# Optimization experiments

Hardware: AMD Instinct MI355X
Metric: run time of the kernel (lower is better)

## Reference

```python
import jax, jax.numpy as jnp
import numpy as np

N, FDIM, HDIM, STEPS = 8192, 512, 1024, 50
STRESS, QNOISE = 0.0, 0.1


def setup_inputs() -> dict:
    key = jax.random.key(0)
    ks = jax.random.split(key, 20)
    s = 0.02
    d = {
        "real_antigen": jax.random.normal(ks[0], (N, FDIM), jnp.float32),
        "steps": STEPS,
        # quantum gene projection (self-loop graph -> per-node linear)
        "Wq": jax.random.normal(ks[1], (FDIM, HDIM), jnp.float32) * s,
        "bq": jnp.zeros((HDIM,), jnp.float32),
        # denoise_0: Linear(h,h) ReLU Linear(h,f)
        "W01": jax.random.normal(ks[2], (HDIM, HDIM), jnp.float32) * s,
        "b01": jnp.zeros((HDIM,), jnp.float32),
        "W02": jax.random.normal(ks[3], (HDIM, FDIM), jnp.float32) * s,
        "b02": jnp.zeros((FDIM,), jnp.float32),
        # denoise_1: Linear(h,h) Tanh Linear(h,f)
        "W11": jax.random.normal(ks[4], (HDIM, HDIM), jnp.float32) * s,
        "b11": jnp.zeros((HDIM,), jnp.float32),
        "W12": jax.random.normal(ks[5], (HDIM, FDIM), jnp.float32) * s,
        "b12": jnp.zeros((FDIM,), jnp.float32),
        # interference_net: Linear(2f,h) GELU Linear(h,f)
        "Wi1": jax.random.normal(ks[6], (2 * FDIM, HDIM), jnp.float32) * s,
        "bi1": jnp.zeros((HDIM,), jnp.float32),
        "Wi2": jax.random.normal(ks[7], (HDIM, FDIM), jnp.float32) * s,
        "bi2": jnp.zeros((FDIM,), jnp.float32),
        # quantum state scalars
        "alpha_amp": jnp.asarray(np.cos(0.6), jnp.float32),
        "beta_amp": jnp.asarray(np.sin(0.6), jnp.float32),
        "phase_cos": jnp.asarray(np.cos(0.3), jnp.float32),
    }
    return d


def reference(real_antigen, steps, Wq, bq, W01, b01, W02, b02, W11, b11,
              W12, b12, Wi1, bi1, Wi2, bi2, alpha_amp, beta_amp, phase_cos):
    sched = jnp.linspace(1e-4, 0.02, 100, dtype=jnp.float32)
    decoherence_rate = jnp.float32(0.1 + STRESS * 0.5)
    decay = jnp.exp(-decoherence_rate)
    # quantum probabilities (fixed amplitudes during the rollout)
    a2, b2 = alpha_amp ** 2, beta_amp ** 2
    p0 = a2 / (a2 + b2)
    p1 = b2 / (a2 + b2)
    sp0, sp1 = jnp.sqrt(p0), jnp.sqrt(p1)
    base_key = jax.random.key(1)
    x0 = jax.random.normal(jax.random.fold_in(base_key, 10_000), real_antigen.shape, jnp.float32)

    def step(carry, t):
        x, coh = carry
        qf = jax.nn.relu(x @ Wq + bq)                           # [N, H]
        d0 = jax.nn.relu(qf @ W01 + b01) @ W02 + b02            # [N, F]
        d1 = jnp.tanh(qf @ W11 + b11) @ W12 + b12               # [N, F]
        inter_in = jnp.concatenate([d0, d1], axis=-1)           # [N, 2F]
        interf = jax.nn.gelu(inter_in @ Wi1 + bi1, approximate=False) @ Wi2 + bi2
        qi = 2.0 * jnp.sqrt(p0 * p1) * phase_cos * coh          # scalar interference
        denoised = sp0 * d0 + sp1 * d1 + qi * interf
        alpha = jnp.maximum(1.0 - sched[t], 1e-8)
        alpha_prev = jnp.where(t > 0, 1.0 - sched[jnp.maximum(t - 1, 0)], 1.0)
        sqrt_1ma = jnp.sqrt(jnp.maximum(1.0 - alpha, 1e-8))
        x_new = (x - (1.0 - alpha) / sqrt_1ma * denoised) / jnp.sqrt(alpha)
        sigma = jnp.sqrt(jnp.maximum((1.0 - alpha_prev) / (1.0 - alpha) * (1.0 - alpha / alpha_prev), 0.0))
        noise = jax.random.normal(jax.random.fold_in(base_key, t), x.shape, jnp.float32)
        x_new = jnp.where(t > 0, x_new + (sigma + QNOISE * jnp.abs(qi)) * noise, x_new)
        return (x_new, coh * decay), None

    ts = jnp.arange(int(steps) - 1, -1, -1, dtype=jnp.int32)
    (x, _), _ = jax.lax.scan(step, (x0, jnp.float32(1.0)), ts)
    # quantum measurement: collapse to |0> with probability p0
    u = jax.random.uniform(jax.random.fold_in(base_key, 99_999), (), jnp.float32)
    dream = jnp.where(u < p0, 0.7 * x + 0.3 * real_antigen, x)
    return dream
```

## Files before the change

kernel.cpp:

```cpp
#include <hip/hip_runtime.h>
#include <stdint.h>
#include <math.h>


typedef __bf16 bf16x8 __attribute__((ext_vector_type(8)));
typedef float floatx4 __attribute__((ext_vector_type(4)));

__host__ __device__ inline void tf2x32(uint32_t k0, uint32_t k1,
                                       uint32_t x0, uint32_t x1,
                                       uint32_t& o0, uint32_t& o1) {
  uint32_t ks2 = k0 ^ k1 ^ 0x1BD11BDAu;
#define TF_R(r) { x0 += x1; x1 = (x1 << (r)) | (x1 >> (32 - (r))); x1 ^= x0; }
  x0 += k0; x1 += k1;
  TF_R(13) TF_R(15) TF_R(26) TF_R(6)
  x0 += k1;  x1 += ks2 + 1u;
  TF_R(17) TF_R(29) TF_R(16) TF_R(24)
  x0 += ks2; x1 += k0 + 2u;
  TF_R(13) TF_R(15) TF_R(26) TF_R(6)
  x0 += k0;  x1 += k1 + 3u;
  TF_R(17) TF_R(29) TF_R(16) TF_R(24)
  x0 += k1;  x1 += ks2 + 4u;
  TF_R(13) TF_R(15) TF_R(26) TF_R(6)
  x0 += ks2; x1 += k0 + 5u;
#undef TF_R
  o0 = x0; o1 = x1;
}

__device__ inline float erfinv_f32(float x) {
  float w = -log1pf(-x * x);
  float p;
  if (w < 5.0f) {
    w = w - 2.5f;
    p = 2.81022636e-08f;
    p = fmaf(p, w, 3.43273939e-07f);
    p = fmaf(p, w, -3.5233877e-06f);
    p = fmaf(p, w, -4.39150654e-06f);
    p = fmaf(p, w, 0.00021858087f);
    p = fmaf(p, w, -0.00125372503f);
    p = fmaf(p, w, -0.00417768164f);
    p = fmaf(p, w, 0.246640727f);
    p = fmaf(p, w, 1.50140941f);
  } else {
    w = sqrtf(w) - 3.0f;
    p = -0.000200214257f;
    p = fmaf(p, w, 0.000100950558f);
    p = fmaf(p, w, 0.00134934322f);
    p = fmaf(p, w, -0.00367342844f);
    p = fmaf(p, w, 0.00573950773f);
    p = fmaf(p, w, -0.0076224613f);
    p = fmaf(p, w, 0.00943887047f);
    p = fmaf(p, w, 1.00167406f);
    p = fmaf(p, w, 2.83297682f);
  }
  return p * x;
}

__device__ inline float tf_normal(uint32_t k0, uint32_t k1, uint32_t i) {
  uint32_t o0, o1;
  tf2x32(k0, k1, 0u, i, o0, o1);
  uint32_t bits = o0 ^ o1;
  float f = __uint_as_float(0x3F800000u | (bits >> 9)) - 1.0f;
  float u = f * 2.0f + (-0.99999994f);
  u = fmaxf(-0.99999994f, u);
  return 1.41421356f * erfinv_f32(u);
}

__device__ inline unsigned short f2bf(float f) {
  uint32_t u = __float_as_uint(f);
  u += 0x7FFFu + ((u >> 16) & 1u);
  return (unsigned short)(u >> 16);
}
__device__ inline float bf2f(unsigned short h) {
  return __uint_as_float(((uint32_t)h) << 16);
}

__global__ __launch_bounds__(256)
void transpose_bf16_kernel(const float* __restrict__ W,
                           unsigned short* __restrict__ Wt, int K, int N) {
  __shared__ float tile[32][33];
  int kb = blockIdx.x * 32, nb = blockIdx.y * 32;
  int tx = threadIdx.x & 31, ty = threadIdx.x >> 5;
#pragma unroll
  for (int i = 0; i < 32; i += 8)
    tile[ty + i][tx] = W[(size_t)(kb + ty + i) * N + nb + tx];
  __syncthreads();
#pragma unroll
  for (int i = 0; i < 32; i += 8)
    Wt[(size_t)(nb + ty + i) * K + kb + tx] = f2bf(tile[tx][ty + i]);
}

__device__ __forceinline__ void gemm_core_db(
    const unsigned short* __restrict__ A0, const unsigned short* __restrict__ A1,
    int lda0, int lda1, int K0, int Ktot,
    const unsigned short* __restrict__ Bt,
    int row0, int col0,
    unsigned short (*As)[128 * 32], unsigned short (*Bs)[128 * 32],
    floatx4 (&acc)[4][4]) {
  const int tid = threadIdx.x;
  const int wave = tid >> 6, lane = tid & 63;
  const int wr = wave >> 1, wc = wave & 1;
  const int lrow = lane >> 2;
  const int lk = (lane & 3) * 8;
  const int fm = lane & 15, quad = lane >> 4;

  auto issue = [&](int kt, int buf) {
    const int k0 = kt * 32;
    const unsigned short* Ap; int kOff, lda;
    if (k0 < K0) { Ap = A0; kOff = k0; lda = lda0; }
    else         { Ap = A1; kOff = k0 - K0; lda = lda1; }
#pragma unroll
    for (int r = 0; r < 2; r++) {
      int srow = r * 64 + wave * 16 + lrow;
      __builtin_amdgcn_global_load_lds(
          (const __attribute__((address_space(1))) uint32_t*)
              (Ap + (size_t)(row0 + srow) * lda + kOff + lk),
          (__attribute__((address_space(3))) uint32_t*)(&As[buf][srow * 32 + lk]),
          16, 0, 0);
      __builtin_amdgcn_global_load_lds(
          (const __attribute__((address_space(1))) uint32_t*)
              (Bt + (size_t)(col0 + srow) * Ktot + k0 + lk),
          (__attribute__((address_space(3))) uint32_t*)(&Bs[buf][srow * 32 + lk]),
          16, 0, 0);
    }
  };

  const int nk = Ktot >> 5;
  issue(0, 0);
  for (int k = 0; k < nk; k++) {
    const int cur = k & 1;
    if (k + 1 < nk) {
      issue(k + 1, cur ^ 1);
      asm volatile("s_waitcnt vmcnt(4)\ns_barrier" ::: "memory");
    } else {
      asm volatile("s_waitcnt vmcnt(0)\ns_barrier" ::: "memory");
    }
    bf16x8 a[4], b[4];
#pragma unroll
    for (int u = 0; u < 4; u++)
      a[u] = *(const bf16x8*)(&As[cur][(wr * 64 + u * 16 + fm) * 32 + quad * 8]);
#pragma unroll
    for (int v = 0; v < 4; v++)
      b[v] = *(const bf16x8*)(&Bs[cur][(wc * 64 + v * 16 + fm) * 32 + quad * 8]);
#pragma unroll
    for (int u = 0; u < 4; u++)
#pragma unroll
      for (int v = 0; v < 4; v++)
        acc[u][v] = __builtin_amdgcn_mfma_f32_16x16x32_bf16(a[u], b[v],
                                                            acc[u][v], 0, 0, 0);
    asm volatile("s_barrier" ::: "memory");
  }
}

__device__ __forceinline__ void swizzled_block(int& row0, int& col0) {
  int id = blockIdx.x + gridDim.x * blockIdx.y;
  row0 = (id & 63) << 7;
  col0 = (id >> 6) << 7;
}

template<int ACT>
__global__ __launch_bounds__(256)
void mfma_gemm(const unsigned short* __restrict__ A0,
               const unsigned short* __restrict__ A1,
               int lda0, int lda1, int K0, int Ktot,
               const unsigned short* __restrict__ Bt,
               const float* __restrict__ bias0,
               const float* __restrict__ bias1, int nsplit,
               unsigned short* __restrict__ C0,
               unsigned short* __restrict__ C1, int ldc) {
  __shared__ unsigned short As[2][128 * 32];
  __shared__ unsigned short Bs[2][128 * 32];
  int row0, col0;
  swizzled_block(row0, col0);
  floatx4 acc[4][4];
#pragma unroll
  for (int u = 0; u < 4; u++)
#pragma unroll
    for (int v = 0; v < 4; v++) acc[u][v] = (floatx4){0.f, 0.f, 0.f, 0.f};
  gemm_core_db(A0, A1, lda0, lda1, K0, Ktot, Bt, row0, col0, As, Bs, acc);

  const int lane = threadIdx.x & 63, wave = threadIdx.x >> 6;
  const int wr = wave >> 1, wc = wave & 1;
  const int fm = lane & 15, quad = lane >> 4;
  const bool side = (ACT == 4) && (col0 >= nsplit);
  const float* bias = side ? bias1 : bias0;
  unsigned short* C = side ? C1 : C0;
  const int cbase = col0 - (side ? nsplit : 0);
#pragma unroll
  for (int v = 0; v < 4; v++) {
    int col = cbase + wc * 64 + v * 16 + fm;
    float bv = bias[col];
#pragma unroll
    for (int u = 0; u < 4; u++) {
      int rbase = row0 + wr * 64 + u * 16 + quad * 4;
#pragma unroll
      for (int r = 0; r < 4; r++) {
        float val = acc[u][v][r] + bv;
        if (ACT == 1) val = fmaxf(val, 0.0f);
        if (ACT == 2) val = tanhf(val);
        if (ACT == 3) val = 0.5f * val * (1.0f + erff(val * 0.70710678118654752f));
        if (ACT == 4) val = side ? tanhf(val) : fmaxf(val, 0.0f);
        C[(size_t)(rbase + r) * ldc + col] = f2bf(val);
      }
    }
  }
}

__global__ __launch_bounds__(256)
void mfma_gemm_pair(const unsigned short* __restrict__ Aa,
                    const unsigned short* __restrict__ Ab,
                    const unsigned short* __restrict__ Bta,
                    const unsigned short* __restrict__ Btb,
                    const float* __restrict__ biasa,
                    const float* __restrict__ biasb,
                    unsigned short* __restrict__ Ca,
                    unsigned short* __restrict__ Cb,
                    int Ktot, int ldc) {
  __shared__ unsigned short As[2][128 * 32];
  __shared__ unsigned short Bs[2][128 * 32];
  const int z = blockIdx.z;
  const unsigned short* A = z ? Ab : Aa;
  const unsigned short* Bt = z ? Btb : Bta;
  const float* bias = z ? biasb : biasa;
  unsigned short* C = z ? Cb : Ca;
  int row0, col0;
  swizzled_block(row0, col0);
  floatx4 acc[4][4];
#pragma unroll
  for (int u = 0; u < 4; u++)
#pragma unroll
    for (int v = 0; v < 4; v++) acc[u][v] = (floatx4){0.f, 0.f, 0.f, 0.f};
  gemm_core_db(A, A, Ktot, Ktot, Ktot, Ktot, Bt, row0, col0, As, Bs, acc);

  const int lane = threadIdx.x & 63, wave = threadIdx.x >> 6;
  const int wr = wave >> 1, wc = wave & 1;
  const int fm = lane & 15, quad = lane >> 4;
#pragma unroll
  for (int v = 0; v < 4; v++) {
    int col = col0 + wc * 64 + v * 16 + fm;
    float bv = bias[col];
#pragma unroll
    for (int u = 0; u < 4; u++) {
      int rbase = row0 + wr * 64 + u * 16 + quad * 4;
#pragma unroll
      for (int r = 0; r < 4; r++)
        C[(size_t)(rbase + r) * ldc + col] = f2bf(acc[u][v][r] + bv);
    }
  }
}

__global__ void init_normal_kernel(float* __restrict__ x,
                                   unsigned short* __restrict__ xbf,
                                   uint32_t k0, uint32_t k1, int n) {
  int i = blockIdx.x * blockDim.x + threadIdx.x;
  if (i >= n) return;
  float v = tf_normal(k0, k1, (uint32_t)i);
  x[i] = v;
  xbf[i] = f2bf(v);
}

__global__ void update_kernel(float* __restrict__ x,
                              unsigned short* __restrict__ xbf,
                              const unsigned short* __restrict__ d0,
                              const unsigned short* __restrict__ d1,
                              const unsigned short* __restrict__ itf,
                              const float* __restrict__ a_amp,
                              const float* __restrict__ b_amp,
                              const float* __restrict__ ph,
                              float coh, float c1, float sqrt_alpha,
                              float sigma, int add_noise,
                              uint32_t k0, uint32_t k1, int n) {
  int i = blockIdx.x * blockDim.x + threadIdx.x;
  if (i >= n) return;
  float aa = a_amp[0], bb = b_amp[0], pc = ph[0];
  float a2 = aa * aa, b2 = bb * bb, s = a2 + b2;
  float p0 = a2 / s, p1 = b2 / s;
  float qi = 2.0f * sqrtf(p0 * p1) * pc * coh;
  float den = sqrtf(p0) * bf2f(d0[i]) + sqrtf(p1) * bf2f(d1[i])
            + qi * bf2f(itf[i]);
  float xn = (x[i] - c1 * den) / sqrt_alpha;
  if (add_noise) {
    float nz = tf_normal(k0, k1, (uint32_t)i);
    xn += (sigma + 0.1f * fabsf(qi)) * nz;
  }
  x[i] = xn;
  xbf[i] = f2bf(xn);
}

__global__ void final_kernel(const float* __restrict__ x,
                             const float* __restrict__ real,
                             float* __restrict__ out,
                             const float* __restrict__ a_amp,
                             const float* __restrict__ b_amp,
                             uint32_t k0, uint32_t k1, int n) {
  int i = blockIdx.x * blockDim.x + threadIdx.x;
  if (i >= n) return;
  float aa = a_amp[0], bb = b_amp[0];
  float a2 = aa * aa, b2 = bb * bb;
  float p0 = a2 / (a2 + b2);
  uint32_t o0, o1;
  tf2x32(k0, k1, 0u, 0u, o0, o1);
  uint32_t bits = o0 ^ o1;
  float u = __uint_as_float(0x3F800000u | (bits >> 9)) - 1.0f;
  float xv = x[i];
  out[i] = (u < p0) ? (0.7f * xv + 0.3f * real[i]) : xv;
}

extern "C" void kernel_launch(void* const* d_in, const int* in_sizes, int n_in,
                              void* d_out, int out_size, void* d_ws,
                              size_t ws_size, hipStream_t stream) {
  const float* real = (const float*)d_in[0];
  const float* Wq  = (const float*)d_in[2];
  const float* bq  = (const float*)d_in[3];
  const float* W01 = (const float*)d_in[4];
  const float* b01 = (const float*)d_in[5];
  const float* W02 = (const float*)d_in[6];
  const float* b02 = (const float*)d_in[7];
  const float* W11 = (const float*)d_in[8];
  const float* b11 = (const float*)d_in[9];
  const float* W12 = (const float*)d_in[10];
  const float* b12 = (const float*)d_in[11];
  const float* Wi1 = (const float*)d_in[12];
  const float* bi1 = (const float*)d_in[13];
  const float* Wi2 = (const float*)d_in[14];
  const float* bi2 = (const float*)d_in[15];
  const float* a_amp = (const float*)d_in[16];
  const float* b_amp = (const float*)d_in[17];
  const float* ph    = (const float*)d_in[18];

  const int Nn = 8192, F = 512, H = 1024;
  const int nElem = Nn * F;
  const int NSPLIT_OFF = 1 << 30;

  char* ws = (char*)d_ws;
  float* x = (float*)ws;                                   ws += (size_t)nElem * 4;
  unsigned short* xbf = (unsigned short*)ws;               ws += (size_t)nElem * 2;
  unsigned short* qf  = (unsigned short*)ws;               ws += (size_t)Nn * H * 2;
  unsigned short* h0  = (unsigned short*)ws;               ws += (size_t)Nn * H * 2;
  unsigned short* h1  = (unsigned short*)ws;               ws += (size_t)Nn * H * 2;
  unsigned short* d0  = (unsigned short*)ws;               ws += (size_t)nElem * 2;
  unsigned short* d1  = (unsigned short*)ws;               ws += (size_t)nElem * 2;
  unsigned short* itf = (unsigned short*)ws;               ws += (size_t)nElem * 2;
  unsigned short* Wq_t  = (unsigned short*)ws;             ws += (size_t)F * H * 2;
  unsigned short* WA_t  = (unsigned short*)ws;             ws += (size_t)(2 * H) * H * 2;
  unsigned short* W02_t = (unsigned short*)ws;             ws += (size_t)H * F * 2;
  unsigned short* W12_t = (unsigned short*)ws;             ws += (size_t)H * F * 2;
  unsigned short* Wi1_t = (unsigned short*)ws;             ws += (size_t)(2 * F) * H * 2;
  unsigned short* Wi2_t = (unsigned short*)ws;             ws += (size_t)H * F * 2;

  dim3 tb(256);
  transpose_bf16_kernel<<<dim3(F / 32, H / 32), tb, 0, stream>>>(Wq, Wq_t, F, H);
  transpose_bf16_kernel<<<dim3(H / 32, H / 32), tb, 0, stream>>>(W01, WA_t, H, H);
  transpose_bf16_kernel<<<dim3(H / 32, H / 32), tb, 0, stream>>>(W11, WA_t + (size_t)H * H, H, H);
  transpose_bf16_kernel<<<dim3(H / 32, F / 32), tb, 0, stream>>>(W02, W02_t, H, F);
  transpose_bf16_kernel<<<dim3(H / 32, F / 32), tb, 0, stream>>>(W12, W12_t, H, F);
  transpose_bf16_kernel<<<dim3(2 * F / 32, H / 32), tb, 0, stream>>>(Wi1, Wi1_t, 2 * F, H);
  transpose_bf16_kernel<<<dim3(H / 32, F / 32), tb, 0, stream>>>(Wi2, Wi2_t, H, F);

  uint32_t kx0, kx1; tf2x32(0u, 1u, 0u, 10000u, kx0, kx1);
  init_normal_kernel<<<(nElem + 255) / 256, 256, 0, stream>>>(x, xbf, kx0, kx1, nElem);

  float sched[100];
  for (int i = 0; i < 100; i++)
    sched[i] = (float)(1e-4 + (0.02 - 1e-4) * (double)i / 99.0);
  const float decay = expf(-0.1f);
  float coh = 1.0f;

  dim3 blk(256);
  dim3 g1(H / 128, 64);
  dim3 g2(2 * H / 128, 64);
  dim3 g45(F / 128, 64, 2);
  dim3 g6(H / 128, 64);
  dim3 g7(F / 128, 64);

  for (int j = 0; j < 50; j++) {
    int t = 49 - j;
    mfma_gemm<1><<<g1, blk, 0, stream>>>(xbf, xbf, F, F, F, F, Wq_t,
                                         bq, nullptr, NSPLIT_OFF, qf, nullptr, H);
    mfma_gemm<4><<<g2, blk, 0, stream>>>(qf, qf, H, H, H, H, WA_t,
                                         b01, b11, H, h0, h1, H);
    mfma_gemm_pair<<<g45, blk, 0, stream>>>(h0, h1, W02_t, W12_t, b02, b12,
                                            d0, d1, H, F);
    mfma_gemm<3><<<g6, blk, 0, stream>>>(d0, d1, F, F, F, 2 * F, Wi1_t,
                                         bi1, nullptr, NSPLIT_OFF, qf, nullptr, H);
    mfma_gemm<0><<<g7, blk, 0, stream>>>(qf, qf, H, H, H, H, Wi2_t,
                                         bi2, nullptr, NSPLIT_OFF, itf, nullptr, F);

    float schedt = sched[t];
    float alphaf = fmaxf(1.0f - schedt, 1e-8f);
    float one_m_alpha = 1.0f - alphaf;
    float sqrt_1ma = sqrtf(fmaxf(one_m_alpha, 1e-8f));
    float c1 = one_m_alpha / sqrt_1ma;
    float sqa = sqrtf(alphaf);
    float sigma = 0.0f;
    if (t > 0) {
      float ap = 1.0f - sched[t - 1];
      sigma = sqrtf(fmaxf((1.0f - ap) / one_m_alpha * (1.0f - alphaf / ap), 0.0f));
    }
    uint32_t kt0, kt1; tf2x32(0u, 1u, 0u, (uint32_t)t, kt0, kt1);
    update_kernel<<<(nElem + 255) / 256, 256, 0, stream>>>(
        x, xbf, d0, d1, itf, a_amp, b_amp, ph, coh, c1, sqa, sigma,
        (t > 0) ? 1 : 0, kt0, kt1, nElem);
    coh *= decay;
  }

  uint32_t ku0, ku1; tf2x32(0u, 1u, 0u, 99999u, ku0, ku1);
  final_kernel<<<(nElem + 255) / 256, 256, 0, stream>>>(
      x, real, (float*)d_out, a_amp, b_amp, ku0, ku1, nElem);
}
```

Measured before the change: 9.416 ms.

## Fuse final interference GEMM with the diffusion update epilogue

The last GEMM of each step (Wi2) now applies the denoise/update math directly in its epilogue, so the separate elementwise update kernel and the bf16 itf buffer are removed. The MFMA operand order is swapped so each lane holds four consecutive columns of one row. That lets the epilogue use vectorized loads and stores of x, d0, d1 and xbf. This saves one launch and a full round trip of the interference tensor per step, but the GEMM epilogue now carries the Threefry normal generation, which adds register pressure and ALU work to that kernel.

```diff
diff --git a/kernel.cpp b/kernel.cpp
--- a/kernel.cpp
+++ b/kernel.cpp
@@ -5,6 +5,7 @@
 
 typedef __bf16 bf16x8 __attribute__((ext_vector_type(8)));
 typedef float floatx4 __attribute__((ext_vector_type(4)));
+typedef unsigned int uintx2 __attribute__((ext_vector_type(2)));
 
 __host__ __device__ inline void tf2x32(uint32_t k0, uint32_t k1,
                                        uint32_t x0, uint32_t x1,
@@ -73,6 +74,16 @@
 __device__ inline float bf2f(unsigned short h) {
   return __uint_as_float(((uint32_t)h) << 16);
 }
+__device__ inline uintx2 pack4bf(float a, float b, float c, float d) {
+  uintx2 r;
+  r.x = (uint32_t)f2bf(a) | ((uint32_t)f2bf(b) << 16);
+  r.y = (uint32_t)f2bf(c) | ((uint32_t)f2bf(d) << 16);
+  return r;
+}
+__device__ inline float bfx(uintx2 p, int r) {
+  uint32_t w = (r < 2) ? p.x : p.y;
+  return bf2f((unsigned short)((r & 1) ? (w >> 16) : (w & 0xffffu)));
+}
 
 __global__ __launch_bounds__(256)
 void transpose_bf16_kernel(const float* __restrict__ W,
@@ -89,6 +100,7 @@
     Wt[(size_t)(nb + ty + i) * K + kb + tx] = f2bf(tile[tx][ty + i]);
 }
 
+template<bool SWAP>
 __device__ __forceinline__ void gemm_core_db(
     const unsigned short* __restrict__ A0, const unsigned short* __restrict__ A1,
     int lda0, int lda1, int K0, int Ktot,
@@ -141,12 +153,21 @@
 #pragma unroll
     for (int v = 0; v < 4; v++)
       b[v] = *(const bf16x8*)(&Bs[cur][(wc * 64 + v * 16 + fm) * 32 + quad * 8]);
-#pragma unroll
-    for (int u = 0; u < 4; u++)
+    if constexpr (!SWAP) {
+#pragma unroll
+      for (int u = 0; u < 4; u++)
+#pragma unroll
+        for (int v = 0; v < 4; v++)
+          acc[u][v] = __builtin_amdgcn_mfma_f32_16x16x32_bf16(a[u], b[v],
+                                                              acc[u][v], 0, 0, 0);
+    } else {
 #pragma unroll
       for (int v = 0; v < 4; v++)
-        acc[u][v] = __builtin_amdgcn_mfma_f32_16x16x32_bf16(a[u], b[v],
-                                                            acc[u][v], 0, 0, 0);
+#pragma unroll
+        for (int u = 0; u < 4; u++)
+          acc[v][u] = __builtin_amdgcn_mfma_f32_16x16x32_bf16(b[v], a[u],
+                                                              acc[v][u], 0, 0, 0);
+    }
     asm volatile("s_barrier" ::: "memory");
   }
 }
@@ -176,7 +197,7 @@
   for (int u = 0; u < 4; u++)
 #pragma unroll
     for (int v = 0; v < 4; v++) acc[u][v] = (floatx4){0.f, 0.f, 0.f, 0.f};
-  gemm_core_db(A0, A1, lda0, lda1, K0, Ktot, Bt, row0, col0, As, Bs, acc);
+  gemm_core_db<false>(A0, A1, lda0, lda1, K0, Ktot, Bt, row0, col0, As, Bs, acc);
 
   const int lane = threadIdx.x & 63, wave = threadIdx.x >> 6;
   const int wr = wave >> 1, wc = wave & 1;
@@ -229,7 +250,7 @@
   for (int u = 0; u < 4; u++)
 #pragma unroll
     for (int v = 0; v < 4; v++) acc[u][v] = (floatx4){0.f, 0.f, 0.f, 0.f};
-  gemm_core_db(A, A, Ktot, Ktot, Ktot, Ktot, Bt, row0, col0, As, Bs, acc);
+  gemm_core_db<false>(A, A, Ktot, Ktot, Ktot, Ktot, Bt, row0, col0, As, Bs, acc);
 
   const int lane = threadIdx.x & 63, wave = threadIdx.x >> 6;
   const int wr = wave >> 1, wc = wave & 1;
@@ -244,6 +265,69 @@
 #pragma unroll
       for (int r = 0; r < 4; r++)
         C[(size_t)(rbase + r) * ldc + col] = f2bf(acc[u][v][r] + bv);
+    }
+  }
+}
+
+__global__ __launch_bounds__(256)
+void mfma_gemm_update(const unsigned short* __restrict__ A,
+                      const unsigned short* __restrict__ Bt,
+                      const float* __restrict__ bias,
+                      const unsigned short* __restrict__ d0,
+                      const unsigned short* __restrict__ d1,
+                      float* __restrict__ x,
+                      unsigned short* __restrict__ xbf,
+                      const float* __restrict__ a_amp,
+                      const float* __restrict__ b_amp,
+                      const float* __restrict__ ph,
+                      float coh, float c1, float sqa, float sigma,
+                      int add_noise, uint32_t k0, uint32_t k1) {
+  __shared__ unsigned short As[2][128 * 32];
+  __shared__ unsigned short Bs[2][128 * 32];
+  int row0, col0;
+  swizzled_block(row0, col0);
+  floatx4 acc[4][4];
+#pragma unroll
+  for (int v = 0; v < 4; v++)
+#pragma unroll
+    for (int u = 0; u < 4; u++) acc[v][u] = (floatx4){0.f, 0.f, 0.f, 0.f};
+  gemm_core_db<true>(A, A, 1024, 1024, 1024, 1024, Bt, row0, col0, As, Bs, acc);
+
+  float aa = a_amp[0], bb = b_amp[0], pc = ph[0];
+  float a2 = aa * aa, b2 = bb * bb, s = a2 + b2;
+  float p0 = a2 / s, p1 = b2 / s;
+  float sp0 = sqrtf(p0), sp1 = sqrtf(p1);
+  float qi = 2.0f * sqrtf(p0 * p1) * pc * coh;
+  float nscale = sigma + 0.1f * fabsf(qi);
+  float inv_sqa = 1.0f / sqa;
+
+  const int lane = threadIdx.x & 63, wave = threadIdx.x >> 6;
+  const int wr = wave >> 1, wc = wave & 1;
+  const int fm = lane & 15, quad = lane >> 4;
+  const int cbase = col0 + wc * 64 + quad * 4;
+#pragma unroll
+  for (int v = 0; v < 4; v++) {
+    int colb = cbase + v * 16;
+    floatx4 bv = *(const floatx4*)(bias + colb);
+#pragma unroll
+    for (int u = 0; u < 4; u++) {
+      int row = row0 + wr * 64 + u * 16 + fm;
+      size_t base = (size_t)row * 512 + colb;
+      uintx2 d0p = *(const uintx2*)(d0 + base);
+      uintx2 d1p = *(const uintx2*)(d1 + base);
+      floatx4 xv = *(const floatx4*)(x + base);
+      floatx4 xn;
+#pragma unroll
+      for (int r = 0; r < 4; r++) {
+        float itf = acc[v][u][r] + bv[r];
+        float den = sp0 * bfx(d0p, r) + sp1 * bfx(d1p, r) + qi * itf;
+        float val = (xv[r] - c1 * den) * inv_sqa;
+        if (add_noise)
+          val += nscale * tf_normal(k0, k1, (uint32_t)(base + (size_t)r));
+        xn[r] = val;
+      }
+      *(floatx4*)(x + base) = xn;
+      *(uintx2*)(xbf + base) = pack4bf(xn[0], xn[1], xn[2], xn[3]);
     }
   }
 }
@@ -256,34 +340,6 @@
   float v = tf_normal(k0, k1, (uint32_t)i);
   x[i] = v;
   xbf[i] = f2bf(v);
-}
-
-__global__ void update_kernel(float* __restrict__ x,
-                              unsigned short* __restrict__ xbf,
-                              const unsigned short* __restrict__ d0,
-                              const unsigned short* __restrict__ d1,
-                              const unsigned short* __restrict__ itf,
-                              const float* __restrict__ a_amp,
-                              const float* __restrict__ b_amp,
-                              const float* __restrict__ ph,
-                              float coh, float c1, float sqrt_alpha,
-                              float sigma, int add_noise,
-                              uint32_t k0, uint32_t k1, int n) {
-  int i = blockIdx.x * blockDim.x + threadIdx.x;
-  if (i >= n) return;
-  float aa = a_amp[0], bb = b_amp[0], pc = ph[0];
-  float a2 = aa * aa, b2 = bb * bb, s = a2 + b2;
-  float p0 = a2 / s, p1 = b2 / s;
-  float qi = 2.0f * sqrtf(p0 * p1) * pc * coh;
-  float den = sqrtf(p0) * bf2f(d0[i]) + sqrtf(p1) * bf2f(d1[i])
-            + qi * bf2f(itf[i]);
-  float xn = (x[i] - c1 * den) / sqrt_alpha;
-  if (add_noise) {
-    float nz = tf_normal(k0, k1, (uint32_t)i);
-    xn += (sigma + 0.1f * fabsf(qi)) * nz;
-  }
-  x[i] = xn;
-  xbf[i] = f2bf(xn);
 }
 
 __global__ void final_kernel(const float* __restrict__ x,
@@ -339,7 +395,6 @@
   unsigned short* h1  = (unsigned short*)ws;               ws += (size_t)Nn * H * 2;
   unsigned short* d0  = (unsigned short*)ws;               ws += (size_t)nElem * 2;
   unsigned short* d1  = (unsigned short*)ws;               ws += (size_t)nElem * 2;
-  unsigned short* itf = (unsigned short*)ws;               ws += (size_t)nElem * 2;
   unsigned short* Wq_t  = (unsigned short*)ws;             ws += (size_t)F * H * 2;
   unsigned short* WA_t  = (unsigned short*)ws;             ws += (size_t)(2 * H) * H * 2;
   unsigned short* W02_t = (unsigned short*)ws;             ws += (size_t)H * F * 2;
@@ -382,8 +437,6 @@
                                             d0, d1, H, F);
     mfma_gemm<3><<<g6, blk, 0, stream>>>(d0, d1, F, F, F, 2 * F, Wi1_t,
                                          bi1, nullptr, NSPLIT_OFF, qf, nullptr, H);
-    mfma_gemm<0><<<g7, blk, 0, stream>>>(qf, qf, H, H, H, H, Wi2_t,
-                                         bi2, nullptr, NSPLIT_OFF, itf, nullptr, F);
 
     float schedt = sched[t];
     float alphaf = fmaxf(1.0f - schedt, 1e-8f);
@@ -397,9 +450,9 @@
       sigma = sqrtf(fmaxf((1.0f - ap) / one_m_alpha * (1.0f - alphaf / ap), 0.0f));
     }
     uint32_t kt0, kt1; tf2x32(0u, 1u, 0u, (uint32_t)t, kt0, kt1);
-    update_kernel<<<(nElem + 255) / 256, 256, 0, stream>>>(
-        x, xbf, d0, d1, itf, a_amp, b_amp, ph, coh, c1, sqa, sigma,
-        (t > 0) ? 1 : 0, kt0, kt1, nElem);
+    mfma_gemm_update<<<g7, blk, 0, stream>>>(
+        qf, Wi2_t, bi2, d0, d1, x, xbf, a_amp, b_amp, ph, coh, c1, sqa, sigma,
+        (t > 0) ? 1 : 0, kt0, kt1);
     coh *= decay;
   }
 
```

Result: slower. 15.36 ms (+63.1%).

## Use 8 waves per 128x128 GEMM tile with 32x64 per-wave subtiles

Applied to the files above, without the earlier changes.

Doubles the GEMM block from 256 to 512 threads, arranged as a 4x2 wave grid where each wave computes a 32x64 subtile instead of 64x64. Each thread now issues one global-to-LDS load per operand per K step rather than two, and the vmcnt wait count is adjusted to match. Accumulator registers per thread are halved, allowing more waves in flight to hide latency. In exchange, each wave issues fewer MFMAs per LDS fragment read, so operand reuse drops and the barriers synchronise more waves.

```diff
diff --git a/kernel.cpp b/kernel.cpp
--- a/kernel.cpp
+++ b/kernel.cpp
@@ -95,12 +95,12 @@
     const unsigned short* __restrict__ Bt,
     int row0, int col0,
     unsigned short (*As)[128 * 32], unsigned short (*Bs)[128 * 32],
-    floatx4 (&acc)[4][4]) {
+    floatx4 (&acc)[2][4]) {
   const int tid = threadIdx.x;
   const int wave = tid >> 6, lane = tid & 63;
   const int wr = wave >> 1, wc = wave & 1;
-  const int lrow = lane >> 2;
-  const int lk = (lane & 3) * 8;
+  const int srow = tid >> 2;
+  const int sgr = (tid & 3) * 8;
   const int fm = lane & 15, quad = lane >> 4;
 
   auto issue = [&](int kt, int buf) {
@@ -108,20 +108,16 @@
     const unsigned short* Ap; int kOff, lda;
     if (k0 < K0) { Ap = A0; kOff = k0; lda = lda0; }
     else         { Ap = A1; kOff = k0 - K0; lda = lda1; }
-#pragma unroll
-    for (int r = 0; r < 2; r++) {
-      int srow = r * 64 + wave * 16 + lrow;
-      __builtin_amdgcn_global_load_lds(
-          (const __attribute__((address_space(1))) uint32_t*)
-              (Ap + (size_t)(row0 + srow) * lda + kOff + lk),
-          (__attribute__((address_space(3))) uint32_t*)(&As[buf][srow * 32 + lk]),
-          16, 0, 0);
-      __builtin_amdgcn_global_load_lds(
-          (const __attribute__((address_space(1))) uint32_t*)
-              (Bt + (size_t)(col0 + srow) * Ktot + k0 + lk),
-          (__attribute__((address_space(3))) uint32_t*)(&Bs[buf][srow * 32 + lk]),
-          16, 0, 0);
-    }
+    __builtin_amdgcn_global_load_lds(
+        (const __attribute__((address_space(1))) uint32_t*)
+            (Ap + (size_t)(row0 + srow) * lda + kOff + sgr),
+        (__attribute__((address_space(3))) uint32_t*)(&As[buf][srow * 32 + sgr]),
+        16, 0, 0);
+    __builtin_amdgcn_global_load_lds(
+        (const __attribute__((address_space(1))) uint32_t*)
+            (Bt + (size_t)(col0 + srow) * Ktot + k0 + sgr),
+        (__attribute__((address_space(3))) uint32_t*)(&Bs[buf][srow * 32 + sgr]),
+        16, 0, 0);
   };
 
   const int nk = Ktot >> 5;
@@ -130,23 +126,23 @@
     const int cur = k & 1;
     if (k + 1 < nk) {
       issue(k + 1, cur ^ 1);
-      asm volatile("s_waitcnt vmcnt(4)\ns_barrier" ::: "memory");
+      asm volatile("s_waitcnt vmcnt(2)\ns_barrier" ::: "memory");
     } else {
       asm volatile("s_waitcnt vmcnt(0)\ns_barrier" ::: "memory");
     }
-    bf16x8 a[4], b[4];
-#pragma unroll
-    for (int u = 0; u < 4; u++)
-      a[u] = *(const bf16x8*)(&As[cur][(wr * 64 + u * 16 + fm) * 32 + quad * 8]);
-#pragma unroll
-    for (int v = 0; v < 4; v++)
-      b[v] = *(const bf16x8*)(&Bs[cur][(wc * 64 + v * 16 + fm) * 32 + quad * 8]);
-#pragma unroll
-    for (int u = 0; u < 4; u++)
-#pragma unroll
-      for (int v = 0; v < 4; v++)
-        acc[u][v] = __builtin_amdgcn_mfma_f32_16x16x32_bf16(a[u], b[v],
-                                                            acc[u][v], 0, 0, 0);
+    bf16x8 a[2], b[4];
+#pragma unroll
+    for (int tm = 0; tm < 2; tm++)
+      a[tm] = *(const bf16x8*)(&As[cur][(wr * 32 + tm * 16 + fm) * 32 + quad * 8]);
+#pragma unroll
+    for (int tn = 0; tn < 4; tn++)
+      b[tn] = *(const bf16x8*)(&Bs[cur][(wc * 64 + tn * 16 + fm) * 32 + quad * 8]);
+#pragma unroll
+    for (int tm = 0; tm < 2; tm++)
+#pragma unroll
+      for (int tn = 0; tn < 4; tn++)
+        acc[tm][tn] = __builtin_amdgcn_mfma_f32_16x16x32_bf16(a[tm], b[tn],
+                                                              acc[tm][tn], 0, 0, 0);
     asm volatile("s_barrier" ::: "memory");
   }
 }
@@ -158,7 +154,7 @@
 }
 
 template<int ACT>
-__global__ __launch_bounds__(256)
+__global__ __launch_bounds__(512, 4)
 void mfma_gemm(const unsigned short* __restrict__ A0,
                const unsigned short* __restrict__ A1,
                int lda0, int lda1, int K0, int Ktot,
@@ -171,11 +167,11 @@
   __shared__ unsigned short Bs[2][128 * 32];
   int row0, col0;
   swizzled_block(row0, col0);
-  floatx4 acc[4][4];
-#pragma unroll
-  for (int u = 0; u < 4; u++)
-#pragma unroll
-    for (int v = 0; v < 4; v++) acc[u][v] = (floatx4){0.f, 0.f, 0.f, 0.f};
+  floatx4 acc[2][4];
+#pragma unroll
+  for (int tm = 0; tm < 2; tm++)
+#pragma unroll
+    for (int tn = 0; tn < 4; tn++) acc[tm][tn] = (floatx4){0.f, 0.f, 0.f, 0.f};
   gemm_core_db(A0, A1, lda0, lda1, K0, Ktot, Bt, row0, col0, As, Bs, acc);
 
   const int lane = threadIdx.x & 63, wave = threadIdx.x >> 6;
@@ -186,15 +182,15 @@
   unsigned short* C = side ? C1 : C0;
   const int cbase = col0 - (side ? nsplit : 0);
 #pragma unroll
-  for (int v = 0; v < 4; v++) {
-    int col = cbase + wc * 64 + v * 16 + fm;
+  for (int tn = 0; tn < 4; tn++) {
+    int col = cbase + wc * 64 + tn * 16 + fm;
     float bv = bias[col];
 #pragma unroll
-    for (int u = 0; u < 4; u++) {
-      int rbase = row0 + wr * 64 + u * 16 + quad * 4;
+    for (int tm = 0; tm < 2; tm++) {
+      int rbase = row0 + wr * 32 + tm * 16 + quad * 4;
 #pragma unroll
       for (int r = 0; r < 4; r++) {
-        float val = acc[u][v][r] + bv;
+        float val = acc[tm][tn][r] + bv;
         if (ACT == 1) val = fmaxf(val, 0.0f);
         if (ACT == 2) val = tanhf(val);
         if (ACT == 3) val = 0.5f * val * (1.0f + erff(val * 0.70710678118654752f));
@@ -205,7 +201,7 @@
   }
 }
 
-__global__ __launch_bounds__(256)
+__global__ __launch_bounds__(512, 4)
 void mfma_gemm_pair(const unsigned short* __restrict__ Aa,
                     const unsigned short* __restrict__ Ab,
                     const unsigned short* __restrict__ Bta,
@@ -224,26 +220,26 @@
   unsigned short* C = z ? Cb : Ca;
   int row0, col0;
   swizzled_block(row0, col0);
-  floatx4 acc[4][4];
-#pragma unroll
-  for (int u = 0; u < 4; u++)
-#pragma unroll
-    for (int v = 0; v < 4; v++) acc[u][v] = (floatx4){0.f, 0.f, 0.f, 0.f};
+  floatx4 acc[2][4];
+#pragma unroll
+  for (int tm = 0; tm < 2; tm++)
+#pragma unroll
+    for (int tn = 0; tn < 4; tn++) acc[tm][tn] = (floatx4){0.f, 0.f, 0.f, 0.f};
   gemm_core_db(A, A, Ktot, Ktot, Ktot, Ktot, Bt, row0, col0, As, Bs, acc);
 
   const int lane = threadIdx.x & 63, wave = threadIdx.x >> 6;
   const int wr = wave >> 1, wc = wave & 1;
   const int fm = lane & 15, quad = lane >> 4;
 #pragma unroll
-  for (int v = 0; v < 4; v++) {
-    int col = col0 + wc * 64 + v * 16 + fm;
+  for (int tn = 0; tn < 4; tn++) {
+    int col = col0 + wc * 64 + tn * 16 + fm;
     float bv = bias[col];
 #pragma unroll
-    for (int u = 0; u < 4; u++) {
-      int rbase = row0 + wr * 64 + u * 16 + quad * 4;
+    for (int tm = 0; tm < 2; tm++) {
+      int rbase = row0 + wr * 32 + tm * 16 + quad * 4;
 #pragma unroll
       for (int r = 0; r < 4; r++)
-        C[(size_t)(rbase + r) * ldc + col] = f2bf(acc[u][v][r] + bv);
+        C[(size_t)(rbase + r) * ldc + col] = f2bf(acc[tm][tn][r] + bv);
     }
   }
 }
@@ -365,7 +361,7 @@
   const float decay = expf(-0.1f);
   float coh = 1.0f;
 
-  dim3 blk(256);
+  dim3 blk(512);
   dim3 g1(H / 128, 64);
   dim3 g2(2 * H / 128, 64);
   dim3 g45(F / 128, 64, 2);
```

Result: faster. 8.881 ms (-5.7%).
